# Optimization experiments

Hardware: AMD Instinct MI355X
Metric: run time of the kernel (lower is better)

## Reference

```python
import jax, jax.numpy as jnp
import numpy as np

N = 1_000_000      # nodes
E = 8_000_000      # edges per relation
IN, HID, OUT = 25, 10, 5
GAT_SLOPE = 0.2    # GATv2Conv negative_slope default
ACT_SLOPE = 0.1    # module's LeakyReLU(0.1)


def setup_inputs() -> dict:
    key = jax.random.key(0)
    ks = jax.random.split(key, 40)
    d = {}
    d["x"] = jax.random.normal(ks[0], (N, IN), dtype=jnp.float32)
    for i, s in enumerate("psv"):
        d[f"edge_index_{s}"] = jax.random.randint(ks[1 + i], (2, E), 0, N, dtype=jnp.int32)
    # GATv2Conv params per relation: lin_l (source), lin_r (target), attention vec, bias
    k = 4
    for s in "psv":
        d[f"Wl_{s}"] = jax.random.normal(ks[k], (IN, OUT), jnp.float32) * 0.2; k += 1
        d[f"Wr_{s}"] = jax.random.normal(ks[k], (IN, OUT), jnp.float32) * 0.2; k += 1
        d[f"att_{s}"] = jax.random.normal(ks[k], (OUT,), jnp.float32) * 0.2; k += 1
        d[f"b_{s}"] = jnp.zeros((OUT,), jnp.float32)
    # projection: Linear(15,10) -> LeakyReLU(0.1) -> Linear(10,5)
    d["Wp1"] = jax.random.normal(ks[k], (3 * OUT, 2 * OUT), jnp.float32) * 0.2; k += 1
    d["bp1"] = jnp.zeros((2 * OUT,), jnp.float32)
    d["Wp2"] = jax.random.normal(ks[k], (2 * OUT, OUT), jnp.float32) * 0.2; k += 1
    d["bp2"] = jnp.zeros((OUT,), jnp.float32)
    # classifier: Linear(5,5) -> LeakyReLU(0.1) -> Linear(5,2)
    d["Wc1"] = jax.random.normal(ks[k], (OUT, OUT), jnp.float32) * 0.2; k += 1
    d["bc1"] = jnp.zeros((OUT,), jnp.float32)
    d["Wc2"] = jax.random.normal(ks[k], (OUT, 2), jnp.float32) * 0.2; k += 1
    d["bc2"] = jnp.zeros((2,), jnp.float32)
    return d


def lrelu(v, slope):
    return jnp.where(v >= 0, v, slope * v)


def gatv2_conv(x, edge_index, Wl, Wr, att, bias):
    """Single-head GATv2Conv with self-loops (PyG defaults)."""
    loops = jnp.arange(N, dtype=edge_index.dtype)
    src = jnp.concatenate([edge_index[0], loops])  # message sources j
    dst = jnp.concatenate([edge_index[1], loops])  # message targets i
    xl = x @ Wl  # [N, OUT] source transform (also message value)
    xr = x @ Wr  # [N, OUT] target transform
    # per-edge attention logits: a^T LeakyReLU(xl[j] + xr[i])
    e = lrelu(xl[src] + xr[dst], GAT_SLOPE) @ att  # [E+N]
    # segment softmax over incoming edges of each target node
    m = jax.ops.segment_max(e, dst, num_segments=N)
    ex = jnp.exp(e - m[dst])
    denom = jax.ops.segment_sum(ex, dst, num_segments=N)
    alpha = ex / denom[dst]
    out = jax.ops.segment_sum(alpha[:, None] * xl[src], dst, num_segments=N)
    return out + bias


def reference(x, edge_index_p, edge_index_s, edge_index_v,
              Wl_p, Wr_p, att_p, b_p,
              Wl_s, Wr_s, att_s, b_s,
              Wl_v, Wr_v, att_v, b_v,
              Wp1, bp1, Wp2, bp2, Wc1, bc1, Wc2, bc2):
    xp = lrelu(gatv2_conv(x, edge_index_p, Wl_p, Wr_p, att_p, b_p), ACT_SLOPE)
    xs = lrelu(gatv2_conv(x, edge_index_s, Wl_s, Wr_s, att_s, b_s), ACT_SLOPE)
    xv = lrelu(gatv2_conv(x, edge_index_v, Wl_v, Wr_v, att_v, b_v), ACT_SLOPE)
    h = jnp.concatenate([xp, xs, xv], axis=1)            # [N, 15]
    h = lrelu(h @ Wp1 + bp1, ACT_SLOPE) @ Wp2 + bp2      # projection (dropout=0)
    h = lrelu(h @ Wc1 + bc1, ACT_SLOPE) @ Wc2 + bc2      # classifier
    return h  # [N, 2]
```

## Files before the change

### kernel.cpp

```cpp
#include <hip/hip_runtime.h>

static constexpr int KIN  = 25;
static constexpr int KOUT = 5;
static constexpr int NBLK = 512;
static constexpr int BTH  = 1024;
static constexpr int BSH  = 9;
static constexpr int NPB  = 1 << BSH;
static constexpr int NBH  = 2048;
static constexpr int BROW = NBH + 1;
static constexpr int CAP  = 5120;

__global__ __launch_bounds__(256) void k_node1(
    const float* __restrict__ x,
    const float* __restrict__ Wl, const float* __restrict__ Wr,
    float* __restrict__ xl8, float* __restrict__ xr5, int n)
{
    __shared__ float sWl[KIN * KOUT];
    __shared__ float sWr[KIN * KOUT];
    __shared__ float sx[256 * KIN];

    const int tid = threadIdx.x;
    if (tid < KIN * KOUT) { sWl[tid] = Wl[tid]; sWr[tid] = Wr[tid]; }

    const int base = blockIdx.x * 256;
    const int cnt  = min(256, n - base);
    const size_t xbase = (size_t)base * KIN;
    for (int i = tid; i < cnt * KIN; i += 256) sx[i] = x[xbase + i];
    __syncthreads();

    if (tid >= cnt) return;
    const int node = base + tid;

    float xls[KOUT] = {0.f, 0.f, 0.f, 0.f, 0.f};
    float xrs[KOUT] = {0.f, 0.f, 0.f, 0.f, 0.f};
    const float* xp = &sx[tid * KIN];
#pragma unroll
    for (int i = 0; i < KIN; ++i) {
        const float xv = xp[i];
#pragma unroll
        for (int o = 0; o < KOUT; ++o) {
            xls[o] += xv * sWl[i * KOUT + o];
            xrs[o] += xv * sWr[i * KOUT + o];
        }
    }

    const size_t n8 = (size_t)node * 8;
    float4 v4;
    v4.x = xls[0]; v4.y = xls[1]; v4.z = xls[2]; v4.w = xls[3];
    *(float4*)(xl8 + n8) = v4;
    xl8[n8 + 4] = xls[4];
    const size_t n5 = (size_t)node * 5;
#pragma unroll
    for (int o = 0; o < KOUT; ++o) xr5[n5 + o] = xrs[o];
}

__global__ __launch_bounds__(BTH) void k_histnode(
    const int* __restrict__ d0p, const int* __restrict__ d1p,
    const int* __restrict__ d2p, int E, int NB, int* __restrict__ hist3,
    const float* __restrict__ x,
    const float* __restrict__ Wl0, const float* __restrict__ Wr0,
    const float* __restrict__ Wl1, const float* __restrict__ Wr1,
    const float* __restrict__ Wl2, const float* __restrict__ Wr2,
    float* __restrict__ xl8, float* __restrict__ xr5, int n, int NNB)
{
    __shared__ float smem[7424];
    const int y = blockIdx.y, bx = blockIdx.x, tid = threadIdx.x;

    if (bx < NBLK) {
        int* h = (int*)smem;
        const int* dst = (y == 0) ? d0p : (y == 1 ? d1p : d2p);
        int* hist_blk = hist3 + (size_t)y * NBLK * NBH;
        for (int i = tid; i < NB; i += BTH) h[i] = 0;
        __syncthreads();
        const int chunk = (((E + NBLK - 1) / NBLK) + 3) & ~3;
        const int eb = bx * chunk, ee = min(E, eb + chunk);
        const int vend = eb + ((ee - eb) & ~3);
        for (int i = eb + tid * 4; i < vend; i += BTH * 4) {
            const int4 d4 = *(const int4*)(dst + i);
            atomicAdd(&h[d4.x >> BSH], 1);
            atomicAdd(&h[d4.y >> BSH], 1);
            atomicAdd(&h[d4.z >> BSH], 1);
            atomicAdd(&h[d4.w >> BSH], 1);
        }
        for (int i = vend + tid; i < ee; i += BTH)
            atomicAdd(&h[dst[i] >> BSH], 1);
        __syncthreads();
        for (int i = tid; i < NB; i += BTH) hist_blk[bx * NBH + i] = h[i];
        return;
    }

    if (y != 0) return;
    const int g = bx - NBLK;
    if (g >= NNB) return;

    float* sW = smem;
    float* sx = smem + 768;
    if (tid < KIN * KOUT) {
        sW[tid]       = Wl0[tid]; sW[125 + tid] = Wr0[tid];
        sW[250 + tid] = Wl1[tid]; sW[375 + tid] = Wr1[tid];
        sW[500 + tid] = Wl2[tid]; sW[625 + tid] = Wr2[tid];
    }

    for (int sub = 0; sub < 4; ++sub) {
        const int base = g * 1024 + sub * 256;
        if (base >= n) break;
        const int cnt = min(256, n - base);
        __syncthreads();
        const size_t xb = (size_t)base * KIN;
        for (int i = tid; i < cnt * KIN; i += BTH) sx[i] = x[xb + i];
        __syncthreads();
        if (tid < cnt) {
            const int node = base + tid;
            float xls[3][KOUT] = {};
            float xrs[3][KOUT] = {};
            const float* xp = &sx[tid * KIN];
#pragma unroll
            for (int i = 0; i < KIN; ++i) {
                const float xv = xp[i];
#pragma unroll
                for (int r = 0; r < 3; ++r)
#pragma unroll
                    for (int o = 0; o < KOUT; ++o) {
                        xls[r][o] += xv * sW[r * 250 + i * KOUT + o];
                        xrs[r][o] += xv * sW[r * 250 + 125 + i * KOUT + o];
                    }
            }
#pragma unroll
            for (int r = 0; r < 3; ++r) {
                const size_t n8 = (size_t)r * n * 8 + (size_t)node * 8;
                float4 v4;
                v4.x = xls[r][0]; v4.y = xls[r][1];
                v4.z = xls[r][2]; v4.w = xls[r][3];
                *(float4*)(xl8 + n8) = v4;
                xl8[n8 + 4] = xls[r][4];
                const size_t n5 = (size_t)r * n * 5 + (size_t)node * 5;
#pragma unroll
                for (int o = 0; o < KOUT; ++o) xr5[n5 + o] = xrs[r][o];
            }
        }
    }
}

__global__ __launch_bounds__(256) void k_sumoffs3(
    int* __restrict__ hist3, int NB, int* __restrict__ totals3)
{
    const int rel = blockIdx.y;
    int* hist_blk = hist3 + (size_t)rel * NBLK * NBH;
    int* totals   = totals3 + rel * NBH;
    const int i = blockIdx.x * 256 + threadIdx.x;
    if (i >= NB) return;
    int s = 0;
    for (int b = 0; b < NBLK; ++b) {
        const int t = hist_blk[b * NBH + i];
        hist_blk[b * NBH + i] = s;
        s += t;
    }
    totals[i] = s;
}

__global__ __launch_bounds__(1024) void k_scan3(
    const int* __restrict__ totals3, int E, int NB, int* __restrict__ base3)
{
    __shared__ int s[1024];
    const int rel = blockIdx.x;
    const int* totals = totals3 + rel * NBH;
    int* base = base3 + rel * BROW;

    const int t = threadIdx.x;
    const int i0 = 2 * t, i1 = 2 * t + 1;
    const int t0 = (i0 < NB) ? totals[i0] : 0;
    const int t1 = (i1 < NB) ? totals[i1] : 0;
    const int pair = t0 + t1;
    s[t] = pair;
    __syncthreads();
    for (int off = 1; off < 1024; off <<= 1) {
        int v = (t >= off) ? s[t - off] : 0;
        __syncthreads();
        s[t] += v;
        __syncthreads();
    }
    const int excl = s[t] - pair;
    base[i0] = excl;
    base[i1] = excl + t0;
    if (t == 1023) base[NBH] = E;
}

__global__ __launch_bounds__(BTH) void k_scatter3(
    const int* __restrict__ s0p, const int* __restrict__ s1p,
    const int* __restrict__ s2p,
    const int* __restrict__ d0p, const int* __restrict__ d1p,
    const int* __restrict__ d2p,
    int E, int NB,
    const int* __restrict__ hist3, const int* __restrict__ base3,
    int* __restrict__ rs3)
{
    __shared__ int cur[NBH];
    const int rel = blockIdx.y, b = blockIdx.x, tid = threadIdx.x;
    const int* src = (rel == 0) ? s0p : (rel == 1 ? s1p : s2p);
    const int* dst = (rel == 0) ? d0p : (rel == 1 ? d1p : d2p);
    const int* hist_blk = hist3 + (size_t)rel * NBLK * NBH;
    const int* base = base3 + rel * BROW;
    int* rs = rs3 + (size_t)rel * E;

    for (int i = tid; i < NB; i += BTH)
        cur[i] = base[i] + hist_blk[b * NBH + i];
    __syncthreads();
    const int chunk = (((E + NBLK - 1) / NBLK) + 3) & ~3;
    const int eb = b * chunk, ee = min(E, eb + chunk);
    const int vend = eb + ((ee - eb) & ~3);
    for (int i = eb + tid * 4; i < vend; i += BTH * 4) {
        const int4 s4 = *(const int4*)(src + i);
        const int4 d4 = *(const int4*)(dst + i);
        int p;
        p = atomicAdd(&cur[d4.x >> BSH], 1); rs[p] = (s4.x << BSH) | (d4.x & (NPB - 1));
        p = atomicAdd(&cur[d4.y >> BSH], 1); rs[p] = (s4.y << BSH) | (d4.y & (NPB - 1));
        p = atomicAdd(&cur[d4.z >> BSH], 1); rs[p] = (s4.z << BSH) | (d4.z & (NPB - 1));
        p = atomicAdd(&cur[d4.w >> BSH], 1); rs[p] = (s4.w << BSH) | (d4.w & (NPB - 1));
    }
    for (int i = vend + tid; i < ee; i += BTH) {
        const int d = dst[i];
        const int pos = atomicAdd(&cur[d >> BSH], 1);
        rs[pos] = (src[i] << BSH) | (d & (NPB - 1));
    }
}

template <int NREL>
__global__ __launch_bounds__(256) void k_gather4(
    const int* __restrict__ rs3, const int* __restrict__ base3,
    const float* __restrict__ xl8a, const float* __restrict__ xr5a,
    const float* __restrict__ at0, const float* __restrict__ at1,
    const float* __restrict__ at2,
    const float* __restrict__ bi0, const float* __restrict__ bi1,
    const float* __restrict__ bi2,
    float* __restrict__ xouta, int n, int E, int NB)
{
    __shared__ float acc[NPB][6];
    __shared__ float xrw[NPB * 5];
    __shared__ int   cur[NPB];
    __shared__ int   sorted[CAP];
    __shared__ int   sc[256];

    const int bx  = blockIdx.x;
    const int rel = (NREL == 1) ? 0 : bx / NB;
    const int bkt = (NREL == 1) ? bx : bx % NB;

    const int*   rs   = rs3 + (size_t)rel * E;
    const int*   base = base3 + rel * BROW;
    const float* xl8  = xl8a + (size_t)rel * 8 * n;
    const float* xr5  = xr5a + (size_t)rel * 5 * n;
    const float* att  = (rel == 0) ? at0 : (rel == 1 ? at1 : at2);
    const float* bias = (rel == 0) ? bi0 : (rel == 1 ? bi1 : bi2);
    float*       xout = xouta + (size_t)rel * 5 * n;

    const int tid = threadIdx.x;
    const int node0 = bkt << BSH;
    const int nn = min(NPB, n - node0);

    for (int i = tid; i < NPB * 6; i += 256) ((float*)acc)[i] = 0.f;
    for (int i = tid; i < nn * 5; i += 256) xrw[i] = xr5[(size_t)node0 * 5 + i];
    for (int i = tid; i < NPB; i += 256) cur[i] = 0;
    __syncthreads();

    const float a0 = att[0], a1 = att[1], a2 = att[2], a3 = att[3], a4 = att[4];
    const int eb = base[bkt], ee = base[bkt + 1];
    const int seg = ee - eb;

    if (seg > 0 && seg <= CAP) {
        for (int i = eb + tid; i < ee; i += 256)
            atomicAdd(&cur[rs[i] & (NPB - 1)], 1);
        __syncthreads();
        const int h0 = cur[2 * tid], h1 = cur[2 * tid + 1];
        const int pair = h0 + h1;
        sc[tid] = pair;
        __syncthreads();
        for (int off = 1; off < 256; off <<= 1) {
            const int v = (tid >= off) ? sc[tid - off] : 0;
            __syncthreads();
            sc[tid] += v;
            __syncthreads();
        }
        const int excl = sc[tid] - pair;
        cur[2 * tid] = excl;
        cur[2 * tid + 1] = excl + h0;
        __syncthreads();
        for (int i = eb + tid; i < ee; i += 256) {
            const int v = rs[i];
            const int p = atomicAdd(&cur[v & (NPB - 1)], 1);
            sorted[p] = v;
        }
        __syncthreads();
        const int C  = (seg + 255) / 256;
        const int s0 = tid * C;
        const int s1 = min(seg, s0 + C);
        int curdl = -1;
        float A0 = 0.f, A1 = 0.f, A2 = 0.f, A3 = 0.f, A4 = 0.f, A5 = 0.f;
        float xr0 = 0.f, xr1 = 0.f, xr2 = 0.f, xr3 = 0.f, xr4 = 0.f;
        for (int i = s0; i < s1; ++i) {
            const int v  = sorted[i];
            const int dl = v & (NPB - 1);
            const int s  = v >> BSH;
            const size_t s8 = (size_t)s * 8;
            const float4 xs = *(const float4*)(xl8 + s8);
            const float  xs4 = xl8[s8 + 4];
            if (dl != curdl) {
                if (curdl >= 0) {
                    atomicAdd(&acc[curdl][0], A0);
                    atomicAdd(&acc[curdl][1], A1);
                    atomicAdd(&acc[curdl][2], A2);
                    atomicAdd(&acc[curdl][3], A3);
                    atomicAdd(&acc[curdl][4], A4);
                    atomicAdd(&acc[curdl][5], A5);
                }
                curdl = dl;
                A0 = A1 = A2 = A3 = A4 = A5 = 0.f;
                const float* xr = &xrw[dl * 5];
                xr0 = xr[0]; xr1 = xr[1]; xr2 = xr[2]; xr3 = xr[3]; xr4 = xr[4];
            }
            float t, lg = 0.f;
            t = xs.x + xr0; t = (t >= 0.f) ? t : 0.2f * t; lg += t * a0;
            t = xs.y + xr1; t = (t >= 0.f) ? t : 0.2f * t; lg += t * a1;
            t = xs.z + xr2; t = (t >= 0.f) ? t : 0.2f * t; lg += t * a2;
            t = xs.w + xr3; t = (t >= 0.f) ? t : 0.2f * t; lg += t * a3;
            t = xs4  + xr4; t = (t >= 0.f) ? t : 0.2f * t; lg += t * a4;
            const float w = __expf(lg);
            A0 += w * xs.x; A1 += w * xs.y; A2 += w * xs.z;
            A3 += w * xs.w; A4 += w * xs4;  A5 += w;
        }
        if (curdl >= 0) {
            atomicAdd(&acc[curdl][0], A0);
            atomicAdd(&acc[curdl][1], A1);
            atomicAdd(&acc[curdl][2], A2);
            atomicAdd(&acc[curdl][3], A3);
            atomicAdd(&acc[curdl][4], A4);
            atomicAdd(&acc[curdl][5], A5);
        }
        __syncthreads();
    } else if (seg > CAP) {
        for (int i = eb + tid; i < ee; i += 256) {
            const int v  = rs[i];
            const int s  = v >> BSH;
            const int dl = v & (NPB - 1);
            const size_t s8 = (size_t)s * 8;
            const float4 xs = *(const float4*)(xl8 + s8);
            const float  xs4 = xl8[s8 + 4];
            const float* xr = &xrw[dl * 5];
            float t, lg = 0.f;
            t = xs.x + xr[0]; t = (t >= 0.f) ? t : 0.2f * t; lg += t * a0;
            t = xs.y + xr[1]; t = (t >= 0.f) ? t : 0.2f * t; lg += t * a1;
            t = xs.z + xr[2]; t = (t >= 0.f) ? t : 0.2f * t; lg += t * a2;
            t = xs.w + xr[3]; t = (t >= 0.f) ? t : 0.2f * t; lg += t * a3;
            t = xs4  + xr[4]; t = (t >= 0.f) ? t : 0.2f * t; lg += t * a4;
            const float w = __expf(lg);
            atomicAdd(&acc[dl][0], w * xs.x);
            atomicAdd(&acc[dl][1], w * xs.y);
            atomicAdd(&acc[dl][2], w * xs.z);
            atomicAdd(&acc[dl][3], w * xs.w);
            atomicAdd(&acc[dl][4], w * xs4);
            atomicAdd(&acc[dl][5], w);
        }
        __syncthreads();
    } else {
        __syncthreads();
    }

    const float b0 = bias[0], b1 = bias[1], b2 = bias[2], b3 = bias[3], b4 = bias[4];
    for (int l = tid; l < nn; l += 256) {
        const int node = node0 + l;
        const size_t s8 = (size_t)node * 8;
        const float4 xs = *(const float4*)(xl8 + s8);
        const float  xs4 = xl8[s8 + 4];
        const float* xr = &xrw[l * 5];

        float t, lg = 0.f;
        t = xs.x + xr[0]; t = (t >= 0.f) ? t : 0.2f * t; lg += t * a0;
        t = xs.y + xr[1]; t = (t >= 0.f) ? t : 0.2f * t; lg += t * a1;
        t = xs.z + xr[2]; t = (t >= 0.f) ? t : 0.2f * t; lg += t * a2;
        t = xs.w + xr[3]; t = (t >= 0.f) ? t : 0.2f * t; lg += t * a3;
        t = xs4  + xr[4]; t = (t >= 0.f) ? t : 0.2f * t; lg += t * a4;
        const float w = __expf(lg);

        const size_t d5 = (size_t)node * 5;
        const float inv = 1.0f / (acc[l][5] + w);
        float v;
        v = (acc[l][0] + w * xs.x) * inv + b0; xout[d5 + 0] = (v >= 0.f) ? v : 0.1f * v;
        v = (acc[l][1] + w * xs.y) * inv + b1; xout[d5 + 1] = (v >= 0.f) ? v : 0.1f * v;
        v = (acc[l][2] + w * xs.z) * inv + b2; xout[d5 + 2] = (v >= 0.f) ? v : 0.1f * v;
        v = (acc[l][3] + w * xs.w) * inv + b3; xout[d5 + 3] = (v >= 0.f) ? v : 0.1f * v;
        v = (acc[l][4] + w * xs4 ) * inv + b4; xout[d5 + 4] = (v >= 0.f) ? v : 0.1f * v;
    }
}

__global__ __launch_bounds__(256) void k_mlp(
    const float* __restrict__ xp, const float* __restrict__ xs,
    const float* __restrict__ xv,
    const float* __restrict__ Wp1, const float* __restrict__ bp1,
    const float* __restrict__ Wp2, const float* __restrict__ bp2,
    const float* __restrict__ Wc1, const float* __restrict__ bc1,
    const float* __restrict__ Wc2, const float* __restrict__ bc2,
    float* __restrict__ out, int n)
{
    __shared__ float sW[257];
    const int tid = threadIdx.x;
    if (tid < 150) sW[tid] = Wp1[tid];
    if (tid < 10)  sW[150 + tid] = bp1[tid];
    if (tid < 50)  sW[160 + tid] = Wp2[tid];
    if (tid < 5)   sW[210 + tid] = bp2[tid];
    if (tid < 25)  sW[215 + tid] = Wc1[tid];
    if (tid < 5)   sW[240 + tid] = bc1[tid];
    if (tid < 10)  sW[245 + tid] = Wc2[tid];
    if (tid < 2)   sW[255 + tid] = bc2[tid];
    __syncthreads();

    const int node = blockIdx.x * 256 + tid;
    if (node >= n) return;
    const size_t n5 = (size_t)node * KOUT;

    float h[15];
#pragma unroll
    for (int k = 0; k < 5; ++k) {
        h[k]      = xp[n5 + k];
        h[5 + k]  = xs[n5 + k];
        h[10 + k] = xv[n5 + k];
    }

    float t1[10];
#pragma unroll
    for (int o = 0; o < 10; ++o) {
        float a = sW[150 + o];
#pragma unroll
        for (int i = 0; i < 15; ++i) a += h[i] * sW[i * 10 + o];
        t1[o] = (a >= 0.f) ? a : 0.1f * a;
    }

    float t2[5];
#pragma unroll
    for (int o = 0; o < 5; ++o) {
        float a = sW[210 + o];
#pragma unroll
        for (int i = 0; i < 10; ++i) a += t1[i] * sW[160 + i * 5 + o];
        t2[o] = a;
    }

    float t3[5];
#pragma unroll
    for (int o = 0; o < 5; ++o) {
        float a = sW[240 + o];
#pragma unroll
        for (int i = 0; i < 5; ++i) a += t2[i] * sW[215 + i * 5 + o];
        t3[o] = (a >= 0.f) ? a : 0.1f * a;
    }

    float o0 = sW[255], o1 = sW[256];
#pragma unroll
    for (int i = 0; i < 5; ++i) {
        o0 += t3[i] * sW[245 + i * 2 + 0];
        o1 += t3[i] * sW[245 + i * 2 + 1];
    }
    out[(size_t)node * 2 + 0] = o0;
    out[(size_t)node * 2 + 1] = o1;
}

extern "C" void kernel_launch(void* const* d_in, const int* in_sizes, int n_in,
                              void* d_out, int out_size, void* d_ws, size_t ws_size,
                              hipStream_t stream)
{
    const float* x = (const float*)d_in[0];
    const int n = in_sizes[0] / KIN;
    const int E = in_sizes[1] / 2;
    const int NB = (n + NPB - 1) >> BSH;

    const int* ei[3] = { (const int*)d_in[1], (const int*)d_in[2], (const int*)d_in[3] };
    const float *Wl[3], *Wr[3], *att[3], *bias[3];
    for (int r = 0; r < 3; ++r) {
        const int base = 4 + r * 4;
        Wl[r]   = (const float*)d_in[base + 0];
        Wr[r]   = (const float*)d_in[base + 1];
        att[r]  = (const float*)d_in[base + 2];
        bias[r] = (const float*)d_in[base + 3];
    }
    const float* Wp1 = (const float*)d_in[16];
    const float* bp1 = (const float*)d_in[17];
    const float* Wp2 = (const float*)d_in[18];
    const float* bp2 = (const float*)d_in[19];
    const float* Wc1 = (const float*)d_in[20];
    const float* bc1 = (const float*)d_in[21];
    const float* Wc2 = (const float*)d_in[22];
    const float* bc2 = (const float*)d_in[23];

    const size_t intsA = (size_t)3 * E + 3 * NBH + 3 * BROW;
    const size_t need_A = ((size_t)54 * n + intsA) * 4;
    const bool fused = ws_size >= need_A;

    float* ws   = (float*)d_ws;
    float* xout = ws;
    float* xl8  = ws + (size_t)15 * n;
    float* xr5  = xl8 + (fused ? (size_t)24 * n : (size_t)8 * n);
    int*   rs3  = (int*)(xr5 + (fused ? (size_t)15 * n : (size_t)5 * n));
    int*   totals3 = rs3 + (fused ? (size_t)3 * E : (size_t)E);
    int*   base3   = totals3 + (fused ? 3 * NBH : NBH);
    int*   hist3   = (int*)(xout + (size_t)10 * n);

    const int nb_node = (n + 255) / 256;
    const int nb_cols = (NB + 255) / 256;
    const int NNB     = (n + 1023) / 1024;

    if (fused) {
        k_histnode<<<dim3(NBLK + NNB, 3), BTH, 0, stream>>>(
            ei[0] + E, ei[1] + E, ei[2] + E, E, NB, hist3,
            x, Wl[0], Wr[0], Wl[1], Wr[1], Wl[2], Wr[2], xl8, xr5, n, NNB);
        k_sumoffs3<<<dim3(nb_cols, 3), 256,  0, stream>>>(hist3, NB, totals3);
        k_scan3   <<<3,                1024, 0, stream>>>(totals3, E, NB, base3);
        k_scatter3<<<dim3(NBLK, 3),    BTH,  0, stream>>>(
            ei[0], ei[1], ei[2], ei[0] + E, ei[1] + E, ei[2] + E,
            E, NB, hist3, base3, rs3);
        k_gather4<3><<<3 * NB, 256, 0, stream>>>(
            rs3, base3, xl8, xr5,
            att[0], att[1], att[2], bias[0], bias[1], bias[2],
            xout, n, E, NB);
    } else {
        for (int r = 0; r < 3; ++r) {
            float* xo = xout + (size_t)r * 5 * n;
            k_node1<<<nb_node, 256, 0, stream>>>(x, Wl[r], Wr[r], xl8, xr5, n);
            k_histnode<<<dim3(NBLK, 1), BTH, 0, stream>>>(
                ei[r] + E, ei[r] + E, ei[r] + E, E, NB, hist3,
                x, Wl[r], Wr[r], Wl[r], Wr[r], Wl[r], Wr[r], xl8, xr5, n, 0);
            k_sumoffs3<<<dim3(nb_cols, 1), 256,  0, stream>>>(hist3, NB, totals3);
            k_scan3   <<<1,                1024, 0, stream>>>(totals3, E, NB, base3);
            k_scatter3<<<dim3(NBLK, 1),    BTH,  0, stream>>>(
                ei[r], ei[r], ei[r], ei[r] + E, ei[r] + E, ei[r] + E,
                E, NB, hist3, base3, rs3);
            k_gather4<1><<<NB, 256, 0, stream>>>(
                rs3, base3, xl8, xr5,
                att[r], att[r], att[r], bias[r], bias[r], bias[r],
                xo, n, E, NB);
        }
    }

    k_mlp<<<nb_node, 256, 0, stream>>>(xout, xout + (size_t)5 * n, xout + (size_t)10 * n,
                                       Wp1, bp1, Wp2, bp2, Wc1, bc1, Wc2, bc2,
                                       (float*)d_out, n);
}
```

Before: 1.066 ms.

## Merge all stages into one multi-mode kernel and overlap independent relation stages

Replaces the separate node, histogram, offset, scan, scatter, gather and MLP kernels with a single k_combo kernel whose blocks pick a mode and relation from their block index. Successive launches pair up independent stages from different relations (e.g. scatter of one relation with gather of another) so that little-work phases like the scan and column sums share the GPU with heavy phases. Block size drops from 1024 to 256 threads and the edge chunking grows from 512 to 2048 blocks per relation. Histogram tables now reuse the xout region per relation. The cost is more launches in sequence (9 versus 5), a larger per-thread column walk in the offset pass, and dynamic shared memory sized for the largest mode in each launch.

```diff
diff --git a/kernel.cpp b/kernel.cpp
--- a/kernel.cpp
+++ b/kernel.cpp
@@ -1,349 +1,335 @@
 #include <hip/hip_runtime.h>
 
-static constexpr int KIN  = 25;
-static constexpr int KOUT = 5;
-static constexpr int NBLK = 512;
-static constexpr int BTH  = 1024;
-static constexpr int BSH  = 9;
-static constexpr int NPB  = 1 << BSH;
-static constexpr int NBH  = 2048;
-static constexpr int BROW = NBH + 1;
-static constexpr int CAP  = 5120;
-
-__global__ __launch_bounds__(256) void k_node1(
+static constexpr int KIN   = 25;
+static constexpr int KOUT  = 5;
+static constexpr int NBLK2 = 2048;
+static constexpr int BSH   = 9;
+static constexpr int NPB   = 1 << BSH;
+static constexpr int NBH   = 2048;
+static constexpr int BROW  = NBH + 1;
+static constexpr int CAP   = 5120;
+
+#define M_NONE -1
+#define M_NODE 0
+#define M_HIST 1
+#define M_SUMO 2
+#define M_SCAN 3
+#define M_SCAT 4
+#define M_GATH 5
+#define M_MLP  6
+
+__global__ __launch_bounds__(256) void k_combo(
+    int m0, int r0, int n0, int m1, int r1, int n1, int m2, int r2, int n2,
     const float* __restrict__ x,
-    const float* __restrict__ Wl, const float* __restrict__ Wr,
-    float* __restrict__ xl8, float* __restrict__ xr5, int n)
-{
-    __shared__ float sWl[KIN * KOUT];
-    __shared__ float sWr[KIN * KOUT];
-    __shared__ float sx[256 * KIN];
-
-    const int tid = threadIdx.x;
-    if (tid < KIN * KOUT) { sWl[tid] = Wl[tid]; sWr[tid] = Wr[tid]; }
-
-    const int base = blockIdx.x * 256;
-    const int cnt  = min(256, n - base);
-    const size_t xbase = (size_t)base * KIN;
-    for (int i = tid; i < cnt * KIN; i += 256) sx[i] = x[xbase + i];
-    __syncthreads();
-
-    if (tid >= cnt) return;
-    const int node = base + tid;
-
-    float xls[KOUT] = {0.f, 0.f, 0.f, 0.f, 0.f};
-    float xrs[KOUT] = {0.f, 0.f, 0.f, 0.f, 0.f};
-    const float* xp = &sx[tid * KIN];
-#pragma unroll
-    for (int i = 0; i < KIN; ++i) {
-        const float xv = xp[i];
-#pragma unroll
-        for (int o = 0; o < KOUT; ++o) {
-            xls[o] += xv * sWl[i * KOUT + o];
-            xrs[o] += xv * sWr[i * KOUT + o];
-        }
-    }
-
-    const size_t n8 = (size_t)node * 8;
-    float4 v4;
-    v4.x = xls[0]; v4.y = xls[1]; v4.z = xls[2]; v4.w = xls[3];
-    *(float4*)(xl8 + n8) = v4;
-    xl8[n8 + 4] = xls[4];
-    const size_t n5 = (size_t)node * 5;
-#pragma unroll
-    for (int o = 0; o < KOUT; ++o) xr5[n5 + o] = xrs[o];
-}
-
-__global__ __launch_bounds__(BTH) void k_histnode(
-    const int* __restrict__ d0p, const int* __restrict__ d1p,
-    const int* __restrict__ d2p, int E, int NB, int* __restrict__ hist3,
-    const float* __restrict__ x,
+    const int* __restrict__ e0, const int* __restrict__ e1,
+    const int* __restrict__ e2,
     const float* __restrict__ Wl0, const float* __restrict__ Wr0,
     const float* __restrict__ Wl1, const float* __restrict__ Wr1,
     const float* __restrict__ Wl2, const float* __restrict__ Wr2,
-    float* __restrict__ xl8, float* __restrict__ xr5, int n, int NNB)
+    const float* __restrict__ at0, const float* __restrict__ at1,
+    const float* __restrict__ at2,
+    const float* __restrict__ bi0, const float* __restrict__ bi1,
+    const float* __restrict__ bi2,
+    const float* __restrict__ Wp1, const float* __restrict__ bp1,
+    const float* __restrict__ Wp2, const float* __restrict__ bp2,
+    const float* __restrict__ Wc1, const float* __restrict__ bc1,
+    const float* __restrict__ Wc2, const float* __restrict__ bc2,
+    float* __restrict__ xl8a, float* __restrict__ xr5a,
+    int* __restrict__ rs3, int slotmul,
+    int* __restrict__ totals3, int* __restrict__ base3,
+    float* __restrict__ xout, float* __restrict__ outp,
+    int n, int E, int NB)
 {
-    __shared__ float smem[7424];
-    const int y = blockIdx.y, bx = blockIdx.x, tid = threadIdx.x;
-
-    if (bx < NBLK) {
-        int* h = (int*)smem;
-        const int* dst = (y == 0) ? d0p : (y == 1 ? d1p : d2p);
-        int* hist_blk = hist3 + (size_t)y * NBLK * NBH;
-        for (int i = tid; i < NB; i += BTH) h[i] = 0;
-        __syncthreads();
-        const int chunk = (((E + NBLK - 1) / NBLK) + 3) & ~3;
+    extern __shared__ char smem_raw[];
+    int bx = blockIdx.x;
+    int mode, rel;
+    if (bx < n0)            { mode = m0; rel = r0; }
+    else if (bx < n0 + n1)  { mode = m1; rel = r1; bx -= n0; }
+    else                    { mode = m2; rel = r2; bx -= n0 + n1; }
+    const int tid = threadIdx.x;
+
+    if (mode == M_NODE) {
+        float* sW = (float*)smem_raw;
+        float* sx = sW + 768;
+        if (rel < 0) {
+            if (tid < KIN * KOUT) {
+                sW[tid]       = Wl0[tid]; sW[125 + tid] = Wr0[tid];
+                sW[250 + tid] = Wl1[tid]; sW[375 + tid] = Wr1[tid];
+                sW[500 + tid] = Wl2[tid]; sW[625 + tid] = Wr2[tid];
+            }
+        } else {
+            const float* Wl = (rel == 0) ? Wl0 : (rel == 1 ? Wl1 : Wl2);
+            const float* Wr = (rel == 0) ? Wr0 : (rel == 1 ? Wr1 : Wr2);
+            if (tid < KIN * KOUT) { sW[tid] = Wl[tid]; sW[125 + tid] = Wr[tid]; }
+        }
+        const int NR = (rel < 0) ? 3 : 1;
+        for (int sub = 0; sub < 4; ++sub) {
+            const int base = bx * 1024 + sub * 256;
+            if (base >= n) break;
+            const int cnt = min(256, n - base);
+            __syncthreads();
+            const size_t xb = (size_t)base * KIN;
+            for (int i = tid; i < cnt * KIN; i += 256) sx[i] = x[xb + i];
+            __syncthreads();
+            if (tid < cnt) {
+                const int node = base + tid;
+                float xls[3][KOUT] = {};
+                float xrs[3][KOUT] = {};
+                const float* xp = &sx[tid * KIN];
+#pragma unroll
+                for (int i = 0; i < KIN; ++i) {
+                    const float xv = xp[i];
+                    for (int r = 0; r < NR; ++r)
+#pragma unroll
+                        for (int o = 0; o < KOUT; ++o) {
+                            xls[r][o] += xv * sW[r * 250 + i * KOUT + o];
+                            xrs[r][o] += xv * sW[r * 250 + 125 + i * KOUT + o];
+                        }
+                }
+                for (int r = 0; r < NR; ++r) {
+                    const size_t n8 = (size_t)r * n * 8 + (size_t)node * 8;
+                    float4 v4;
+                    v4.x = xls[r][0]; v4.y = xls[r][1];
+                    v4.z = xls[r][2]; v4.w = xls[r][3];
+                    *(float4*)(xl8a + n8) = v4;
+                    xl8a[n8 + 4] = xls[r][4];
+                    const size_t n5 = (size_t)r * n * 5 + (size_t)node * 5;
+#pragma unroll
+                    for (int o = 0; o < KOUT; ++o) xr5a[n5 + o] = xrs[r][o];
+                }
+            }
+        }
+        return;
+    }
+
+    if (mode == M_HIST) {
+        int* h = (int*)smem_raw;
+        const int* dst = ((rel == 0) ? e0 : (rel == 1) ? e1 : e2) + E;
+        int* hist_blk = (int*)(xout + (size_t)rel * 5 * n);
+        for (int i = tid; i < NB; i += 256) h[i] = 0;
+        __syncthreads();
+        const int chunk = (((E + NBLK2 - 1) / NBLK2) + 3) & ~3;
         const int eb = bx * chunk, ee = min(E, eb + chunk);
         const int vend = eb + ((ee - eb) & ~3);
-        for (int i = eb + tid * 4; i < vend; i += BTH * 4) {
+        for (int i = eb + tid * 4; i < vend; i += 1024) {
             const int4 d4 = *(const int4*)(dst + i);
             atomicAdd(&h[d4.x >> BSH], 1);
             atomicAdd(&h[d4.y >> BSH], 1);
             atomicAdd(&h[d4.z >> BSH], 1);
             atomicAdd(&h[d4.w >> BSH], 1);
         }
-        for (int i = vend + tid; i < ee; i += BTH)
+        for (int i = vend + tid; i < ee; i += 256)
             atomicAdd(&h[dst[i] >> BSH], 1);
         __syncthreads();
-        for (int i = tid; i < NB; i += BTH) hist_blk[bx * NBH + i] = h[i];
-        return;
-    }
-
-    if (y != 0) return;
-    const int g = bx - NBLK;
-    if (g >= NNB) return;
-
-    float* sW = smem;
-    float* sx = smem + 768;
-    if (tid < KIN * KOUT) {
-        sW[tid]       = Wl0[tid]; sW[125 + tid] = Wr0[tid];
-        sW[250 + tid] = Wl1[tid]; sW[375 + tid] = Wr1[tid];
-        sW[500 + tid] = Wl2[tid]; sW[625 + tid] = Wr2[tid];
-    }
-
-    for (int sub = 0; sub < 4; ++sub) {
-        const int base = g * 1024 + sub * 256;
-        if (base >= n) break;
-        const int cnt = min(256, n - base);
-        __syncthreads();
-        const size_t xb = (size_t)base * KIN;
-        for (int i = tid; i < cnt * KIN; i += BTH) sx[i] = x[xb + i];
-        __syncthreads();
-        if (tid < cnt) {
-            const int node = base + tid;
-            float xls[3][KOUT] = {};
-            float xrs[3][KOUT] = {};
-            const float* xp = &sx[tid * KIN];
-#pragma unroll
-            for (int i = 0; i < KIN; ++i) {
-                const float xv = xp[i];
-#pragma unroll
-                for (int r = 0; r < 3; ++r)
-#pragma unroll
-                    for (int o = 0; o < KOUT; ++o) {
-                        xls[r][o] += xv * sW[r * 250 + i * KOUT + o];
-                        xrs[r][o] += xv * sW[r * 250 + 125 + i * KOUT + o];
+        for (int i = tid; i < NB; i += 256) hist_blk[(size_t)bx * NBH + i] = h[i];
+        return;
+    }
+
+    if (mode == M_SUMO) {
+        int* hist_blk = (int*)(xout + (size_t)rel * 5 * n);
+        int* totals   = totals3 + rel * NBH;
+        const int i = bx * 256 + tid;
+        if (i >= NBH) return;
+        if (i >= NB) { totals[i] = 0; return; }
+        int s = 0;
+        for (int b = 0; b < NBLK2; ++b) {
+            const int t = hist_blk[(size_t)b * NBH + i];
+            hist_blk[(size_t)b * NBH + i] = s;
+            s += t;
+        }
+        totals[i] = s;
+        return;
+    }
+
+    if (mode == M_SCAN) {
+        int* s = (int*)smem_raw;
+        const int* totals = totals3 + rel * NBH;
+        int* base = base3 + rel * BROW;
+        int loc[8];
+        int sum = 0;
+#pragma unroll
+        for (int j = 0; j < 8; ++j) { loc[j] = totals[tid * 8 + j]; sum += loc[j]; }
+        s[tid] = sum;
+        __syncthreads();
+        for (int off = 1; off < 256; off <<= 1) {
+            const int v = (tid >= off) ? s[tid - off] : 0;
+            __syncthreads();
+            s[tid] += v;
+            __syncthreads();
+        }
+        int run = s[tid] - sum;
+#pragma unroll
+        for (int j = 0; j < 8; ++j) { base[tid * 8 + j] = run; run += loc[j]; }
+        if (tid == 255) base[NBH] = E;
+        return;
+    }
+
+    if (mode == M_SCAT) {
+        int* cur = (int*)smem_raw;
+        const int* src = (rel == 0) ? e0 : (rel == 1) ? e1 : e2;
+        const int* dst = src + E;
+        const int* hist_blk = (const int*)(xout + (size_t)rel * 5 * n);
+        const int* base = base3 + rel * BROW;
+        int* rs = rs3 + (size_t)rel * slotmul * E;
+
+        for (int i = tid; i < NB; i += 256)
+            cur[i] = base[i] + hist_blk[(size_t)bx * NBH + i];
+        __syncthreads();
+        const int chunk = (((E + NBLK2 - 1) / NBLK2) + 3) & ~3;
+        const int eb = bx * chunk, ee = min(E, eb + chunk);
+        const int vend = eb + ((ee - eb) & ~3);
+        for (int i = eb + tid * 4; i < vend; i += 1024) {
+            const int4 s4 = *(const int4*)(src + i);
+            const int4 d4 = *(const int4*)(dst + i);
+            int p;
+            p = atomicAdd(&cur[d4.x >> BSH], 1); rs[p] = (s4.x << BSH) | (d4.x & (NPB - 1));
+            p = atomicAdd(&cur[d4.y >> BSH], 1); rs[p] = (s4.y << BSH) | (d4.y & (NPB - 1));
+            p = atomicAdd(&cur[d4.z >> BSH], 1); rs[p] = (s4.z << BSH) | (d4.z & (NPB - 1));
+            p = atomicAdd(&cur[d4.w >> BSH], 1); rs[p] = (s4.w << BSH) | (d4.w & (NPB - 1));
+        }
+        for (int i = vend + tid; i < ee; i += 256) {
+            const int d = dst[i];
+            const int p = atomicAdd(&cur[d >> BSH], 1);
+            rs[p] = (src[i] << BSH) | (d & (NPB - 1));
+        }
+        return;
+    }
+
+    if (mode == M_GATH) {
+        float* acc    = (float*)smem_raw;
+        float* xrw    = acc + NPB * 6;
+        int*   cur    = (int*)(xrw + NPB * 5);
+        int*   sorted = cur + NPB;
+        int*   sc     = sorted + CAP;
+
+        const int bkt = bx;
+        const int*   rs   = rs3 + (size_t)rel * slotmul * E;
+        const int*   base = base3 + rel * BROW;
+        const float* xl8  = xl8a + (size_t)rel * slotmul * 8 * n;
+        const float* xr5  = xr5a + (size_t)rel * slotmul * 5 * n;
+        const float* att  = (rel == 0) ? at0 : (rel == 1 ? at1 : at2);
+        const float* bias = (rel == 0) ? bi0 : (rel == 1 ? bi1 : bi2);
+        float*       xo   = xout + (size_t)rel * 5 * n;
+
+        const int node0 = bkt << BSH;
+        const int nn = min(NPB, n - node0);
+
+        for (int i = tid; i < NPB * 6; i += 256) acc[i] = 0.f;
+        for (int i = tid; i < nn * 5; i += 256) xrw[i] = xr5[(size_t)node0 * 5 + i];
+        for (int i = tid; i < NPB; i += 256) cur[i] = 0;
+        __syncthreads();
+
+        const float a0 = att[0], a1 = att[1], a2 = att[2], a3 = att[3], a4 = att[4];
+        const int eb = base[bkt], ee = base[bkt + 1];
+        const int seg = ee - eb;
+
+        if (seg > 0 && seg <= CAP) {
+            for (int i = eb + tid; i < ee; i += 256)
+                atomicAdd(&cur[rs[i] & (NPB - 1)], 1);
+            __syncthreads();
+            const int h0 = cur[2 * tid], h1 = cur[2 * tid + 1];
+            const int pair = h0 + h1;
+            sc[tid] = pair;
+            __syncthreads();
+            for (int off = 1; off < 256; off <<= 1) {
+                const int v = (tid >= off) ? sc[tid - off] : 0;
+                __syncthreads();
+                sc[tid] += v;
+                __syncthreads();
+            }
+            const int excl = sc[tid] - pair;
+            cur[2 * tid] = excl;
+            cur[2 * tid + 1] = excl + h0;
+            __syncthreads();
+            for (int i = eb + tid; i < ee; i += 256) {
+                const int v = rs[i];
+                const int p = atomicAdd(&cur[v & (NPB - 1)], 1);
+                sorted[p] = v;
+            }
+            __syncthreads();
+            const int C  = (seg + 255) / 256;
+            const int s0 = tid * C;
+            const int s1 = min(seg, s0 + C);
+            int curdl = -1;
+            float A0 = 0.f, A1 = 0.f, A2 = 0.f, A3 = 0.f, A4 = 0.f, A5 = 0.f;
+            float xr0 = 0.f, xr1 = 0.f, xr2 = 0.f, xr3 = 0.f, xr4 = 0.f;
+            for (int i = s0; i < s1; ++i) {
+                const int v  = sorted[i];
+                const int dl = v & (NPB - 1);
+                const int s  = v >> BSH;
+                const size_t s8 = (size_t)s * 8;
+                const float4 xs = *(const float4*)(xl8 + s8);
+                const float  xs4 = xl8[s8 + 4];
+                if (dl != curdl) {
+                    if (curdl >= 0) {
+                        atomicAdd(&acc[curdl * 6 + 0], A0);
+                        atomicAdd(&acc[curdl * 6 + 1], A1);
+                        atomicAdd(&acc[curdl * 6 + 2], A2);
+                        atomicAdd(&acc[curdl * 6 + 3], A3);
+                        atomicAdd(&acc[curdl * 6 + 4], A4);
+                        atomicAdd(&acc[curdl * 6 + 5], A5);
                     }
-            }
-#pragma unroll
-            for (int r = 0; r < 3; ++r) {
-                const size_t n8 = (size_t)r * n * 8 + (size_t)node * 8;
-                float4 v4;
-                v4.x = xls[r][0]; v4.y = xls[r][1];
-                v4.z = xls[r][2]; v4.w = xls[r][3];
-                *(float4*)(xl8 + n8) = v4;
-                xl8[n8 + 4] = xls[r][4];
-                const size_t n5 = (size_t)r * n * 5 + (size_t)node * 5;
-#pragma unroll
-                for (int o = 0; o < KOUT; ++o) xr5[n5 + o] = xrs[r][o];
-            }
-        }
-    }
-}
-
-__global__ __launch_bounds__(256) void k_sumoffs3(
-    int* __restrict__ hist3, int NB, int* __restrict__ totals3)
-{
-    const int rel = blockIdx.y;
-    int* hist_blk = hist3 + (size_t)rel * NBLK * NBH;
-    int* totals   = totals3 + rel * NBH;
-    const int i = blockIdx.x * 256 + threadIdx.x;
-    if (i >= NB) return;
-    int s = 0;
-    for (int b = 0; b < NBLK; ++b) {
-        const int t = hist_blk[b * NBH + i];
-        hist_blk[b * NBH + i] = s;
-        s += t;
-    }
-    totals[i] = s;
-}
-
-__global__ __launch_bounds__(1024) void k_scan3(
-    const int* __restrict__ totals3, int E, int NB, int* __restrict__ base3)
-{
-    __shared__ int s[1024];
-    const int rel = blockIdx.x;
-    const int* totals = totals3 + rel * NBH;
-    int* base = base3 + rel * BROW;
-
-    const int t = threadIdx.x;
-    const int i0 = 2 * t, i1 = 2 * t + 1;
-    const int t0 = (i0 < NB) ? totals[i0] : 0;
-    const int t1 = (i1 < NB) ? totals[i1] : 0;
-    const int pair = t0 + t1;
-    s[t] = pair;
-    __syncthreads();
-    for (int off = 1; off < 1024; off <<= 1) {
-        int v = (t >= off) ? s[t - off] : 0;
-        __syncthreads();
-        s[t] += v;
-        __syncthreads();
-    }
-    const int excl = s[t] - pair;
-    base[i0] = excl;
-    base[i1] = excl + t0;
-    if (t == 1023) base[NBH] = E;
-}
-
-__global__ __launch_bounds__(BTH) void k_scatter3(
-    const int* __restrict__ s0p, const int* __restrict__ s1p,
-    const int* __restrict__ s2p,
-    const int* __restrict__ d0p, const int* __restrict__ d1p,
-    const int* __restrict__ d2p,
-    int E, int NB,
-    const int* __restrict__ hist3, const int* __restrict__ base3,
-    int* __restrict__ rs3)
-{
-    __shared__ int cur[NBH];
-    const int rel = blockIdx.y, b = blockIdx.x, tid = threadIdx.x;
-    const int* src = (rel == 0) ? s0p : (rel == 1 ? s1p : s2p);
-    const int* dst = (rel == 0) ? d0p : (rel == 1 ? d1p : d2p);
-    const int* hist_blk = hist3 + (size_t)rel * NBLK * NBH;
-    const int* base = base3 + rel * BROW;
-    int* rs = rs3 + (size_t)rel * E;
-
-    for (int i = tid; i < NB; i += BTH)
-        cur[i] = base[i] + hist_blk[b * NBH + i];
-    __syncthreads();
-    const int chunk = (((E + NBLK - 1) / NBLK) + 3) & ~3;
-    const int eb = b * chunk, ee = min(E, eb + chunk);
-    const int vend = eb + ((ee - eb) & ~3);
-    for (int i = eb + tid * 4; i < vend; i += BTH * 4) {
-        const int4 s4 = *(const int4*)(src + i);
-        const int4 d4 = *(const int4*)(dst + i);
-        int p;
-        p = atomicAdd(&cur[d4.x >> BSH], 1); rs[p] = (s4.x << BSH) | (d4.x & (NPB - 1));
-        p = atomicAdd(&cur[d4.y >> BSH], 1); rs[p] = (s4.y << BSH) | (d4.y & (NPB - 1));
-        p = atomicAdd(&cur[d4.z >> BSH], 1); rs[p] = (s4.z << BSH) | (d4.z & (NPB - 1));
-        p = atomicAdd(&cur[d4.w >> BSH], 1); rs[p] = (s4.w << BSH) | (d4.w & (NPB - 1));
-    }
-    for (int i = vend + tid; i < ee; i += BTH) {
-        const int d = dst[i];
-        const int pos = atomicAdd(&cur[d >> BSH], 1);
-        rs[pos] = (src[i] << BSH) | (d & (NPB - 1));
-    }
-}
-
-template <int NREL>
-__global__ __launch_bounds__(256) void k_gather4(
-    const int* __restrict__ rs3, const int* __restrict__ base3,
-    const float* __restrict__ xl8a, const float* __restrict__ xr5a,
-    const float* __restrict__ at0, const float* __restrict__ at1,
-    const float* __restrict__ at2,
-    const float* __restrict__ bi0, const float* __restrict__ bi1,
-    const float* __restrict__ bi2,
-    float* __restrict__ xouta, int n, int E, int NB)
-{
-    __shared__ float acc[NPB][6];
-    __shared__ float xrw[NPB * 5];
-    __shared__ int   cur[NPB];
-    __shared__ int   sorted[CAP];
-    __shared__ int   sc[256];
-
-    const int bx  = blockIdx.x;
-    const int rel = (NREL == 1) ? 0 : bx / NB;
-    const int bkt = (NREL == 1) ? bx : bx % NB;
-
-    const int*   rs   = rs3 + (size_t)rel * E;
-    const int*   base = base3 + rel * BROW;
-    const float* xl8  = xl8a + (size_t)rel * 8 * n;
-    const float* xr5  = xr5a + (size_t)rel * 5 * n;
-    const float* att  = (rel == 0) ? at0 : (rel == 1 ? at1 : at2);
-    const float* bias = (rel == 0) ? bi0 : (rel == 1 ? bi1 : bi2);
-    float*       xout = xouta + (size_t)rel * 5 * n;
-
-    const int tid = threadIdx.x;
-    const int node0 = bkt << BSH;
-    const int nn = min(NPB, n - node0);
-
-    for (int i = tid; i < NPB * 6; i += 256) ((float*)acc)[i] = 0.f;
-    for (int i = tid; i < nn * 5; i += 256) xrw[i] = xr5[(size_t)node0 * 5 + i];
-    for (int i = tid; i < NPB; i += 256) cur[i] = 0;
-    __syncthreads();
-
-    const float a0 = att[0], a1 = att[1], a2 = att[2], a3 = att[3], a4 = att[4];
-    const int eb = base[bkt], ee = base[bkt + 1];
-    const int seg = ee - eb;
-
-    if (seg > 0 && seg <= CAP) {
-        for (int i = eb + tid; i < ee; i += 256)
-            atomicAdd(&cur[rs[i] & (NPB - 1)], 1);
-        __syncthreads();
-        const int h0 = cur[2 * tid], h1 = cur[2 * tid + 1];
-        const int pair = h0 + h1;
-        sc[tid] = pair;
-        __syncthreads();
-        for (int off = 1; off < 256; off <<= 1) {
-            const int v = (tid >= off) ? sc[tid - off] : 0;
-            __syncthreads();
-            sc[tid] += v;
-            __syncthreads();
-        }
-        const int excl = sc[tid] - pair;
-        cur[2 * tid] = excl;
-        cur[2 * tid + 1] = excl + h0;
-        __syncthreads();
-        for (int i = eb + tid; i < ee; i += 256) {
-            const int v = rs[i];
-            const int p = atomicAdd(&cur[v & (NPB - 1)], 1);
-            sorted[p] = v;
-        }
-        __syncthreads();
-        const int C  = (seg + 255) / 256;
-        const int s0 = tid * C;
-        const int s1 = min(seg, s0 + C);
-        int curdl = -1;
-        float A0 = 0.f, A1 = 0.f, A2 = 0.f, A3 = 0.f, A4 = 0.f, A5 = 0.f;
-        float xr0 = 0.f, xr1 = 0.f, xr2 = 0.f, xr3 = 0.f, xr4 = 0.f;
-        for (int i = s0; i < s1; ++i) {
-            const int v  = sorted[i];
-            const int dl = v & (NPB - 1);
-            const int s  = v >> BSH;
-            const size_t s8 = (size_t)s * 8;
+                    curdl = dl;
+                    A0 = A1 = A2 = A3 = A4 = A5 = 0.f;
+                    const float* xr = &xrw[dl * 5];
+                    xr0 = xr[0]; xr1 = xr[1]; xr2 = xr[2]; xr3 = xr[3]; xr4 = xr[4];
+                }
+                float t, lg = 0.f;
+                t = xs.x + xr0; t = (t >= 0.f) ? t : 0.2f * t; lg += t * a0;
+                t = xs.y + xr1; t = (t >= 0.f) ? t : 0.2f * t; lg += t * a1;
+                t = xs.z + xr2; t = (t >= 0.f) ? t : 0.2f * t; lg += t * a2;
+                t = xs.w + xr3; t = (t >= 0.f) ? t : 0.2f * t; lg += t * a3;
+                t = xs4  + xr4; t = (t >= 0.f) ? t : 0.2f * t; lg += t * a4;
+                const float w = __expf(lg);
+                A0 += w * xs.x; A1 += w * xs.y; A2 += w * xs.z;
+                A3 += w * xs.w; A4 += w * xs4;  A5 += w;
+            }
+            if (curdl >= 0) {
+                atomicAdd(&acc[curdl * 6 + 0], A0);
+                atomicAdd(&acc[curdl * 6 + 1], A1);
+                atomicAdd(&acc[curdl * 6 + 2], A2);
+                atomicAdd(&acc[curdl * 6 + 3], A3);
+                atomicAdd(&acc[curdl * 6 + 4], A4);
+                atomicAdd(&acc[curdl * 6 + 5], A5);
+            }
+            __syncthreads();
+        } else if (seg > CAP) {
+            for (int i = eb + tid; i < ee; i += 256) {
+                const int v  = rs[i];
+                const int s  = v >> BSH;
+                const int dl = v & (NPB - 1);
+                const size_t s8 = (size_t)s * 8;
+                const float4 xs = *(const float4*)(xl8 + s8);
+                const float  xs4 = xl8[s8 + 4];
+                const float* xr = &xrw[dl * 5];
+                float t, lg = 0.f;
+                t = xs.x + xr[0]; t = (t >= 0.f) ? t : 0.2f * t; lg += t * a0;
+                t = xs.y + xr[1]; t = (t >= 0.f) ? t : 0.2f * t; lg += t * a1;
+                t = xs.z + xr[2]; t = (t >= 0.f) ? t : 0.2f * t; lg += t * a2;
+                t = xs.w + xr[3]; t = (t >= 0.f) ? t : 0.2f * t; lg += t * a3;
+                t = xs4  + xr[4]; t = (t >= 0.f) ? t : 0.2f * t; lg += t * a4;
+                const float w = __expf(lg);
+                atomicAdd(&acc[dl * 6 + 0], w * xs.x);
+                atomicAdd(&acc[dl * 6 + 1], w * xs.y);
+                atomicAdd(&acc[dl * 6 + 2], w * xs.z);
+                atomicAdd(&acc[dl * 6 + 3], w * xs.w);
+                atomicAdd(&acc[dl * 6 + 4], w * xs4);
+                atomicAdd(&acc[dl * 6 + 5], w);
+            }
+            __syncthreads();
+        } else {
+            __syncthreads();
+        }
+
+        const float b0 = bias[0], b1 = bias[1], b2 = bias[2],
+                    b3 = bias[3], b4 = bias[4];
+        for (int l = tid; l < nn; l += 256) {
+            const int node = node0 + l;
+            const size_t s8 = (size_t)node * 8;
             const float4 xs = *(const float4*)(xl8 + s8);
             const float  xs4 = xl8[s8 + 4];
-            if (dl != curdl) {
-                if (curdl >= 0) {
-                    atomicAdd(&acc[curdl][0], A0);
-                    atomicAdd(&acc[curdl][1], A1);
-                    atomicAdd(&acc[curdl][2], A2);
-                    atomicAdd(&acc[curdl][3], A3);
-                    atomicAdd(&acc[curdl][4], A4);
-                    atomicAdd(&acc[curdl][5], A5);
-                }
-                curdl = dl;
-                A0 = A1 = A2 = A3 = A4 = A5 = 0.f;
-                const float* xr = &xrw[dl * 5];
-                xr0 = xr[0]; xr1 = xr[1]; xr2 = xr[2]; xr3 = xr[3]; xr4 = xr[4];
-            }
-            float t, lg = 0.f;
-            t = xs.x + xr0; t = (t >= 0.f) ? t : 0.2f * t; lg += t * a0;
-            t = xs.y + xr1; t = (t >= 0.f) ? t : 0.2f * t; lg += t * a1;
-            t = xs.z + xr2; t = (t >= 0.f) ? t : 0.2f * t; lg += t * a2;
-            t = xs.w + xr3; t = (t >= 0.f) ? t : 0.2f * t; lg += t * a3;
-            t = xs4  + xr4; t = (t >= 0.f) ? t : 0.2f * t; lg += t * a4;
-            const float w = __expf(lg);
-            A0 += w * xs.x; A1 += w * xs.y; A2 += w * xs.z;
-            A3 += w * xs.w; A4 += w * xs4;  A5 += w;
-        }
-        if (curdl >= 0) {
-            atomicAdd(&acc[curdl][0], A0);
-            atomicAdd(&acc[curdl][1], A1);
-            atomicAdd(&acc[curdl][2], A2);
-            atomicAdd(&acc[curdl][3], A3);
-            atomicAdd(&acc[curdl][4], A4);
-            atomicAdd(&acc[curdl][5], A5);
-        }
-        __syncthreads();
-    } else if (seg > CAP) {
-        for (int i = eb + tid; i < ee; i += 256) {
-            const int v  = rs[i];
-            const int s  = v >> BSH;
-            const int dl = v & (NPB - 1);
-            const size_t s8 = (size_t)s * 8;
-            const float4 xs = *(const float4*)(xl8 + s8);
-            const float  xs4 = xl8[s8 + 4];
-            const float* xr = &xrw[dl * 5];
+            const float* xr = &xrw[l * 5];
+
             float t, lg = 0.f;
             t = xs.x + xr[0]; t = (t >= 0.f) ? t : 0.2f * t; lg += t * a0;
             t = xs.y + xr[1]; t = (t >= 0.f) ? t : 0.2f * t; lg += t * a1;
@@ -351,113 +337,77 @@
             t = xs.w + xr[3]; t = (t >= 0.f) ? t : 0.2f * t; lg += t * a3;
             t = xs4  + xr[4]; t = (t >= 0.f) ? t : 0.2f * t; lg += t * a4;
             const float w = __expf(lg);
-            atomicAdd(&acc[dl][0], w * xs.x);
-            atomicAdd(&acc[dl][1], w * xs.y);
-            atomicAdd(&acc[dl][2], w * xs.z);
-            atomicAdd(&acc[dl][3], w * xs.w);
-            atomicAdd(&acc[dl][4], w * xs4);
-            atomicAdd(&acc[dl][5], w);
-        }
-        __syncthreads();
-    } else {
-        __syncthreads();
-    }
-
-    const float b0 = bias[0], b1 = bias[1], b2 = bias[2], b3 = bias[3], b4 = bias[4];
-    for (int l = tid; l < nn; l += 256) {
-        const int node = node0 + l;
-        const size_t s8 = (size_t)node * 8;
-        const float4 xs = *(const float4*)(xl8 + s8);
-        const float  xs4 = xl8[s8 + 4];
-        const float* xr = &xrw[l * 5];
-
-        float t, lg = 0.f;
-        t = xs.x + xr[0]; t = (t >= 0.f) ? t : 0.2f * t; lg += t * a0;
-        t = xs.y + xr[1]; t = (t >= 0.f) ? t : 0.2f * t; lg += t * a1;
-        t = xs.z + xr[2]; t = (t >= 0.f) ? t : 0.2f * t; lg += t * a2;
-        t = xs.w + xr[3]; t = (t >= 0.f) ? t : 0.2f * t; lg += t * a3;
-        t = xs4  + xr[4]; t = (t >= 0.f) ? t : 0.2f * t; lg += t * a4;
-        const float w = __expf(lg);
-
-        const size_t d5 = (size_t)node * 5;
-        const float inv = 1.0f / (acc[l][5] + w);
-        float v;
-        v = (acc[l][0] + w * xs.x) * inv + b0; xout[d5 + 0] = (v >= 0.f) ? v : 0.1f * v;
-        v = (acc[l][1] + w * xs.y) * inv + b1; xout[d5 + 1] = (v >= 0.f) ? v : 0.1f * v;
-        v = (acc[l][2] + w * xs.z) * inv + b2; xout[d5 + 2] = (v >= 0.f) ? v : 0.1f * v;
-        v = (acc[l][3] + w * xs.w) * inv + b3; xout[d5 + 3] = (v >= 0.f) ? v : 0.1f * v;
-        v = (acc[l][4] + w * xs4 ) * inv + b4; xout[d5 + 4] = (v >= 0.f) ? v : 0.1f * v;
-    }
-}
-
-__global__ __launch_bounds__(256) void k_mlp(
-    const float* __restrict__ xp, const float* __restrict__ xs,
-    const float* __restrict__ xv,
-    const float* __restrict__ Wp1, const float* __restrict__ bp1,
-    const float* __restrict__ Wp2, const float* __restrict__ bp2,
-    const float* __restrict__ Wc1, const float* __restrict__ bc1,
-    const float* __restrict__ Wc2, const float* __restrict__ bc2,
-    float* __restrict__ out, int n)
-{
-    __shared__ float sW[257];
-    const int tid = threadIdx.x;
-    if (tid < 150) sW[tid] = Wp1[tid];
-    if (tid < 10)  sW[150 + tid] = bp1[tid];
-    if (tid < 50)  sW[160 + tid] = Wp2[tid];
-    if (tid < 5)   sW[210 + tid] = bp2[tid];
-    if (tid < 25)  sW[215 + tid] = Wc1[tid];
-    if (tid < 5)   sW[240 + tid] = bc1[tid];
-    if (tid < 10)  sW[245 + tid] = Wc2[tid];
-    if (tid < 2)   sW[255 + tid] = bc2[tid];
-    __syncthreads();
-
-    const int node = blockIdx.x * 256 + tid;
-    if (node >= n) return;
-    const size_t n5 = (size_t)node * KOUT;
-
-    float h[15];
-#pragma unroll
-    for (int k = 0; k < 5; ++k) {
-        h[k]      = xp[n5 + k];
-        h[5 + k]  = xs[n5 + k];
-        h[10 + k] = xv[n5 + k];
-    }
-
-    float t1[10];
-#pragma unroll
-    for (int o = 0; o < 10; ++o) {
-        float a = sW[150 + o];
-#pragma unroll
-        for (int i = 0; i < 15; ++i) a += h[i] * sW[i * 10 + o];
-        t1[o] = (a >= 0.f) ? a : 0.1f * a;
-    }
-
-    float t2[5];
-#pragma unroll
-    for (int o = 0; o < 5; ++o) {
-        float a = sW[210 + o];
-#pragma unroll
-        for (int i = 0; i < 10; ++i) a += t1[i] * sW[160 + i * 5 + o];
-        t2[o] = a;
-    }
-
-    float t3[5];
-#pragma unroll
-    for (int o = 0; o < 5; ++o) {
-        float a = sW[240 + o];
-#pragma unroll
-        for (int i = 0; i < 5; ++i) a += t2[i] * sW[215 + i * 5 + o];
-        t3[o] = (a >= 0.f) ? a : 0.1f * a;
-    }
-
-    float o0 = sW[255], o1 = sW[256];
-#pragma unroll
-    for (int i = 0; i < 5; ++i) {
-        o0 += t3[i] * sW[245 + i * 2 + 0];
-        o1 += t3[i] * sW[245 + i * 2 + 1];
-    }
-    out[(size_t)node * 2 + 0] = o0;
-    out[(size_t)node * 2 + 1] = o1;
+
+            const size_t d5 = (size_t)node * 5;
+            const float inv = 1.0f / (acc[l * 6 + 5] + w);
+            float v;
+            v = (acc[l * 6 + 0] + w * xs.x) * inv + b0; xo[d5 + 0] = (v >= 0.f) ? v : 0.1f * v;
+            v = (acc[l * 6 + 1] + w * xs.y) * inv + b1; xo[d5 + 1] = (v >= 0.f) ? v : 0.1f * v;
+            v = (acc[l * 6 + 2] + w * xs.z) * inv + b2; xo[d5 + 2] = (v >= 0.f) ? v : 0.1f * v;
+            v = (acc[l * 6 + 3] + w * xs.w) * inv + b3; xo[d5 + 3] = (v >= 0.f) ? v : 0.1f * v;
+            v = (acc[l * 6 + 4] + w * xs4 ) * inv + b4; xo[d5 + 4] = (v >= 0.f) ? v : 0.1f * v;
+        }
+        return;
+    }
+
+    if (mode == M_MLP) {
+        float* sW = (float*)smem_raw;
+        if (tid < 150) sW[tid] = Wp1[tid];
+        if (tid < 10)  sW[150 + tid] = bp1[tid];
+        if (tid < 50)  sW[160 + tid] = Wp2[tid];
+        if (tid < 5)   sW[210 + tid] = bp2[tid];
+        if (tid < 25)  sW[215 + tid] = Wc1[tid];
+        if (tid < 5)   sW[240 + tid] = bc1[tid];
+        if (tid < 10)  sW[245 + tid] = Wc2[tid];
+        if (tid < 2)   sW[255 + tid] = bc2[tid];
+        __syncthreads();
+
+        const int node = bx * 256 + tid;
+        if (node >= n) return;
+        const size_t n5 = (size_t)node * KOUT;
+
+        float h[15];
+#pragma unroll
+        for (int k = 0; k < 5; ++k) {
+            h[k]      = xout[n5 + k];
+            h[5 + k]  = xout[(size_t)5 * n + n5 + k];
+            h[10 + k] = xout[(size_t)10 * n + n5 + k];
+        }
+
+        float t1[10];
+#pragma unroll
+        for (int o = 0; o < 10; ++o) {
+            float a = sW[150 + o];
+#pragma unroll
+            for (int i = 0; i < 15; ++i) a += h[i] * sW[i * 10 + o];
+            t1[o] = (a >= 0.f) ? a : 0.1f * a;
+        }
+        float t2[5];
+#pragma unroll
+        for (int o = 0; o < 5; ++o) {
+            float a = sW[210 + o];
+#pragma unroll
+            for (int i = 0; i < 10; ++i) a += t1[i] * sW[160 + i * 5 + o];
+            t2[o] = a;
+        }
+        float t3[5];
+#pragma unroll
+        for (int o = 0; o < 5; ++o) {
+            float a = sW[240 + o];
+#pragma unroll
+            for (int i = 0; i < 5; ++i) a += t2[i] * sW[215 + i * 5 + o];
+            t3[o] = (a >= 0.f) ? a : 0.1f * a;
+        }
+        float o0 = sW[255], o1 = sW[256];
+#pragma unroll
+        for (int i = 0; i < 5; ++i) {
+            o0 += t3[i] * sW[245 + i * 2 + 0];
+            o1 += t3[i] * sW[245 + i * 2 + 1];
+        }
+        outp[(size_t)node * 2 + 0] = o0;
+        outp[(size_t)node * 2 + 1] = o1;
+        return;
+    }
 }
 
 extern "C" void kernel_launch(void* const* d_in, const int* in_sizes, int n_in,
@@ -490,6 +440,7 @@
     const size_t intsA = (size_t)3 * E + 3 * NBH + 3 * BROW;
     const size_t need_A = ((size_t)54 * n + intsA) * 4;
     const bool fused = ws_size >= need_A;
+    const int slotmul = fused ? 1 : 0;
 
     float* ws   = (float*)d_ws;
     float* xout = ws;
@@ -497,46 +448,43 @@
     float* xr5  = xl8 + (fused ? (size_t)24 * n : (size_t)8 * n);
     int*   rs3  = (int*)(xr5 + (fused ? (size_t)15 * n : (size_t)5 * n));
     int*   totals3 = rs3 + (fused ? (size_t)3 * E : (size_t)E);
-    int*   base3   = totals3 + (fused ? 3 * NBH : NBH);
-    int*   hist3   = (int*)(xout + (size_t)10 * n);
-
-    const int nb_node = (n + 255) / 256;
-    const int nb_cols = (NB + 255) / 256;
-    const int NNB     = (n + 1023) / 1024;
+    int*   base3   = totals3 + 3 * NBH;
+
+    const int NNB  = (n + 1023) / 1024;
+    const int NMLP = (n + 255) / 256;
+
+    const size_t L_NODE = 28672, L_TAB = 8192, L_SCAN = 1024,
+                 L_GATH = 46080, L_MLP = 1056;
+
+#define ARGS x, ei[0], ei[1], ei[2],                                          \
+    Wl[0], Wr[0], Wl[1], Wr[1], Wl[2], Wr[2],                                 \
+    att[0], att[1], att[2], bias[0], bias[1], bias[2],                        \
+    Wp1, bp1, Wp2, bp2, Wc1, bc1, Wc2, bc2,                                   \
+    xl8, xr5, rs3, slotmul, totals3, base3, xout, (float*)d_out, n, E, NB
+#define L(m0,r0,n0,m1,r1,n1,m2,r2,n2,lds)                                     \
+    k_combo<<<(n0)+(n1)+(n2), 256, (lds), stream>>>(                          \
+        m0,r0,n0, m1,r1,n1, m2,r2,n2, ARGS)
 
     if (fused) {
-        k_histnode<<<dim3(NBLK + NNB, 3), BTH, 0, stream>>>(
-            ei[0] + E, ei[1] + E, ei[2] + E, E, NB, hist3,
-            x, Wl[0], Wr[0], Wl[1], Wr[1], Wl[2], Wr[2], xl8, xr5, n, NNB);
-        k_sumoffs3<<<dim3(nb_cols, 3), 256,  0, stream>>>(hist3, NB, totals3);
-        k_scan3   <<<3,                1024, 0, stream>>>(totals3, E, NB, base3);
-        k_scatter3<<<dim3(NBLK, 3),    BTH,  0, stream>>>(
-            ei[0], ei[1], ei[2], ei[0] + E, ei[1] + E, ei[2] + E,
-            E, NB, hist3, base3, rs3);
-        k_gather4<3><<<3 * NB, 256, 0, stream>>>(
-            rs3, base3, xl8, xr5,
-            att[0], att[1], att[2], bias[0], bias[1], bias[2],
-            xout, n, E, NB);
+        L(M_NODE,-1,NNB,   M_HIST,0,NBLK2,  M_NONE,0,0,  L_NODE);
+        L(M_HIST,1,NBLK2,  M_SUMO,0,8,      M_NONE,0,0,  L_TAB);
+        L(M_HIST,2,NBLK2,  M_SCAN,0,1,      M_NONE,0,0,  L_TAB);
+        L(M_SCAT,0,NBLK2,  M_SUMO,1,8,      M_NONE,0,0,  L_TAB);
+        L(M_SUMO,2,8,      M_SCAN,1,1,      M_NONE,0,0,  L_SCAN);
+        L(M_GATH,0,NB,     M_SCAT,1,NBLK2,  M_SCAN,2,1,  L_GATH);
+        L(M_GATH,1,NB,     M_SCAT,2,NBLK2,  M_NONE,0,0,  L_GATH);
+        L(M_GATH,2,NB,     M_NONE,0,0,      M_NONE,0,0,  L_GATH);
+        L(M_MLP,0,NMLP,    M_NONE,0,0,      M_NONE,0,0,  L_MLP);
     } else {
         for (int r = 0; r < 3; ++r) {
-            float* xo = xout + (size_t)r * 5 * n;
-            k_node1<<<nb_node, 256, 0, stream>>>(x, Wl[r], Wr[r], xl8, xr5, n);
-            k_histnode<<<dim3(NBLK, 1), BTH, 0, stream>>>(
-                ei[r] + E, ei[r] + E, ei[r] + E, E, NB, hist3,
-                x, Wl[r], Wr[r], Wl[r], Wr[r], Wl[r], Wr[r], xl8, xr5, n, 0);
-            k_sumoffs3<<<dim3(nb_cols, 1), 256,  0, stream>>>(hist3, NB, totals3);
-            k_scan3   <<<1,                1024, 0, stream>>>(totals3, E, NB, base3);
-            k_scatter3<<<dim3(NBLK, 1),    BTH,  0, stream>>>(
-                ei[r], ei[r], ei[r], ei[r] + E, ei[r] + E, ei[r] + E,
-                E, NB, hist3, base3, rs3);
-            k_gather4<1><<<NB, 256, 0, stream>>>(
-                rs3, base3, xl8, xr5,
-                att[r], att[r], att[r], bias[r], bias[r], bias[r],
-                xo, n, E, NB);
-        }
-    }
-
-    k_mlp<<<nb_node, 256, 0, stream>>>(xout, xout + (size_t)5 * n, xout + (size_t)10 * n,
-                                       Wp1, bp1, Wp2, bp2, Wc1, bc1, Wc2, bc2,
-                                       (float*)d_out, n);
+            L(M_NODE,r,NNB,   M_HIST,r,NBLK2, M_NONE,0,0, L_NODE);
+            L(M_SUMO,r,8,     M_NONE,0,0,     M_NONE,0,0, L_TAB);
+            L(M_SCAN,r,1,     M_NONE,0,0,     M_NONE,0,0, L_SCAN);
+            L(M_SCAT,r,NBLK2, M_NONE,0,0,     M_NONE,0,0, L_TAB);
+            L(M_GATH,r,NB,    M_NONE,0,0,     M_NONE,0,0, L_GATH);
+        }
+        L(M_MLP,0,NMLP, M_NONE,0,0, M_NONE,0,0, L_MLP);
+    }
+#undef L
+#undef ARGS
 }
```

Result: slower. 1.274 ms (+19.6%).
